# Performance work log

Measured on AMD Instinct MI355X. Metric: run time of the kernel, lower is better.

The kernel has to match this reference:

```python
import jax, jax.numpy as jnp
import numpy as np

N, E, NG = 10000, 160000, 64
HID, HEADS = 256, 4
NEG_SLOPE = 0.2


def setup_inputs() -> dict:
    key = jax.random.key(0)
    ks = jax.random.split(key, 20)
    s = 0.1
    inp = {
        "atom_features": jax.random.normal(ks[0], (N, 23), jnp.float32),
        "edge_index": jax.random.randint(ks[1], (2, E), 0, N),
        "batch": jnp.sort(jax.random.randint(ks[2], (N,), 0, NG)),
        "W1": jax.random.normal(ks[3], (23, HEADS * HID), jnp.float32) * s,
        "as1": jax.random.normal(ks[4], (HEADS, HID), jnp.float32) * s,
        "ad1": jax.random.normal(ks[5], (HEADS, HID), jnp.float32) * s,
        "b1": jnp.zeros((HEADS * HID,), jnp.float32),
        "W2": jax.random.normal(ks[6], (HEADS * HID, HEADS * HID), jnp.float32) * s,
        "as2": jax.random.normal(ks[7], (HEADS, HID), jnp.float32) * s,
        "ad2": jax.random.normal(ks[8], (HEADS, HID), jnp.float32) * s,
        "b2": jnp.zeros((HEADS * HID,), jnp.float32),
        "W3": jax.random.normal(ks[9], (HEADS * HID, HID), jnp.float32) * s,
        "as3": jax.random.normal(ks[10], (1, HID), jnp.float32) * s,
        "ad3": jax.random.normal(ks[11], (1, HID), jnp.float32) * s,
        "b3": jnp.zeros((HID,), jnp.float32),
        # MLP head
        "fc1_w": jax.random.normal(ks[12], (HID, HID // 2), jnp.float32) * s,
        "fc1_b": jnp.zeros((HID // 2,), jnp.float32),
        "fc2_w": jax.random.normal(ks[13], (HID // 2, 1), jnp.float32) * s,
        "fc2_b": jnp.zeros((1,), jnp.float32),
    }
    return inp


def gat_layer(x, W, att_src, att_dst, bias, src, dst, heads, ch):
    n = x.shape[0]
    h = (x @ W).reshape(n, heads, ch)                      # [N,H,C]
    a_s = jnp.sum(h * att_src, axis=-1)                    # [N,H]
    a_d = jnp.sum(h * att_dst, axis=-1)                    # [N,H]
    logits = jax.nn.leaky_relu(a_s[src] + a_d[dst], NEG_SLOPE)  # [E',H]
    m = jax.ops.segment_max(logits, dst, num_segments=n)
    m = jnp.where(jnp.isfinite(m), m, 0.0)
    e = jnp.exp(logits - m[dst])
    denom = jax.ops.segment_sum(e, dst, num_segments=n)
    alpha = e / (denom[dst] + 1e-16)                       # segment softmax over incoming edges
    out = jax.ops.segment_sum(alpha[:, :, None] * h[src], dst, num_segments=n)
    return out.reshape(n, heads * ch) + bias


def reference(atom_features, edge_index, batch,
              W1, as1, ad1, b1, W2, as2, ad2, b2, W3, as3, ad3, b3,
              fc1_w, fc1_b, fc2_w, fc2_b):
    n = atom_features.shape[0]
    loops = jnp.arange(n)
    src = jnp.concatenate([edge_index[0], loops])   # PyG GATConv adds self-loops
    dst = jnp.concatenate([edge_index[1], loops])

    x = jax.nn.elu(gat_layer(atom_features, W1, as1, ad1, b1, src, dst, HEADS, HID))
    x = jax.nn.elu(gat_layer(x, W2, as2, ad2, b2, src, dst, HEADS, HID))
    x = jax.nn.elu(gat_layer(x, W3, as3, ad3, b3, src, dst, 1, HID))
    # dropout: eval mode (training=False) -> identity

    # global mean pool over molecules
    sums = jax.ops.segment_sum(x, batch, num_segments=NG)
    counts = jax.ops.segment_sum(jnp.ones((n,), x.dtype), batch, num_segments=NG)
    features = sums / jnp.maximum(counts, 1.0)[:, None]    # [NG, HID]

    hmid = jax.nn.relu(features @ fc1_w + fc1_b)
    validity = hmid @ fc2_w + fc2_b                        # [NG, 1]
    return validity, features
```

## Files before the change

kernel.cpp:

```cpp
#include <hip/hip_runtime.h>
#include <hip/hip_bf16.h>
#include <math.h>

typedef unsigned short ushortT;
typedef __attribute__((ext_vector_type(8))) short short8;
typedef __attribute__((ext_vector_type(4))) float f32x4;

constexpr int NN   = 10000;
constexpr int EE   = 160000;
constexpr int ETOT = EE + NN;
constexpr int NG   = 64;
constexpr int HID  = 256;
constexpr int HEADS = 4;

__device__ __forceinline__ ushortT f2bf(float x) {
    __hip_bfloat16 h = __float2bfloat16(x);
    return *reinterpret_cast<ushortT*>(&h);
}
__device__ __forceinline__ float bf2f(ushortT x) {
    unsigned u = ((unsigned)x) << 16;
    return __uint_as_float(u);
}

__global__ void edge_count_kernel(const int* __restrict__ ei, int* __restrict__ cnt) {
    int e = blockIdx.x * blockDim.x + threadIdx.x;
    if (e >= ETOT) return;
    int dst = (e < EE) ? ei[EE + e] : (e - EE);
    atomicAdd(&cnt[dst], 1);
}

__global__ void scan_kernel(const int* __restrict__ cnt, int* __restrict__ row_ptr,
                            int* __restrict__ cursor) {
    __shared__ int part[256];
    int tid = threadIdx.x;
    const int chunk = (NN + 255) / 256;
    int s0 = tid * chunk;
    int s1 = min(NN, s0 + chunk);
    int sum = 0;
    for (int i = s0; i < s1; ++i) sum += cnt[i];
    part[tid] = sum;
    __syncthreads();
    for (int off = 1; off < 256; off <<= 1) {
        int v = (tid >= off) ? part[tid - off] : 0;
        __syncthreads();
        part[tid] += v;
        __syncthreads();
    }
    int run = (tid == 0) ? 0 : part[tid - 1];
    for (int i = s0; i < s1; ++i) {
        row_ptr[i] = run;
        cursor[i]  = run;
        run += cnt[i];
    }
    if (tid == 255) row_ptr[NN] = part[255];
}

__global__ void edge_fill_kernel(const int* __restrict__ ei, int* __restrict__ cursor,
                                 int* __restrict__ col_src) {
    int e = blockIdx.x * blockDim.x + threadIdx.x;
    if (e >= ETOT) return;
    int src, dst;
    if (e < EE) { src = ei[e]; dst = ei[EE + e]; }
    else        { src = dst = e - EE; }
    int pos = atomicAdd(&cursor[dst], 1);
    col_src[pos] = src;
}

__global__ void convert_wt(const float* __restrict__ W, ushortT* __restrict__ Wt,
                           int K, int N, int Kp) {
    __shared__ float t[32][33];
    int n0 = blockIdx.x * 32, k0 = blockIdx.y * 32;
    int tx = threadIdx.x, ty = threadIdx.y;
    for (int i = ty; i < 32; i += 8) {
        int k = k0 + i, n = n0 + tx;
        t[i][tx] = (k < K && n < N) ? W[(size_t)k * N + n] : 0.f;
    }
    __syncthreads();
    for (int i = ty; i < 32; i += 8) {
        int n = n0 + i, kp = k0 + tx;
        if (n < N && kp < Kp) Wt[(size_t)n * Kp + kp] = f2bf(t[tx][i]);
    }
}

__global__ void build_b1p(const float* __restrict__ W1, ushortT* __restrict__ Bp) {
    int idx = blockIdx.x * 256 + threadIdx.x;
    if (idx >= 1024 * 128) return;
    int n = idx >> 7, kp = idx & 127;
    int h = n >> 8, hk = kp >> 5, k = kp & 31;
    float v = (hk == h && k < 23) ? W1[(size_t)k * 1024 + n] : 0.f;
    Bp[idx] = f2bf(v);
}

__global__ void proj_att(const float* __restrict__ W,
                         const float* __restrict__ atts,
                         const float* __restrict__ attd,
                         float* __restrict__ wsv,
                         int K, int heads) {
    const int nout = 2 * heads;
    int gw   = (blockIdx.x * blockDim.x + threadIdx.x) >> 6;
    int lane = threadIdx.x & 63;
    if (gw >= K * nout) return;
    int k = gw / nout, o = gw - k * nout;
    int h = (o >= heads) ? (o - heads) : o;
    const float* att  = ((o >= heads) ? attd : atts) + h * HID;
    const float* wrow = W + (size_t)k * (heads * HID) + h * HID;
    float4 w4 = *(const float4*)(wrow + lane * 4);
    float4 a4 = *(const float4*)(att + lane * 4);
    float s = w4.x * a4.x + w4.y * a4.y + w4.z * a4.z + w4.w * a4.w;
    #pragma unroll
    for (int off = 1; off < 64; off <<= 1) s += __shfl_xor(s, off);
    if (lane == 0) wsv[(size_t)k * nout + o] = s;
}

__global__ void dots1_kernel(const float* __restrict__ atom,
                             const float* __restrict__ wsv1,
                             float* __restrict__ a_s, float* __restrict__ a_d) {
    int n = blockIdx.x * 256 + threadIdx.x;
    if (n >= NN) return;
    float a[8] = {0.f, 0.f, 0.f, 0.f, 0.f, 0.f, 0.f, 0.f};
    #pragma unroll
    for (int k = 0; k < 23; ++k) {
        float x = atom[n * 23 + k];
        #pragma unroll
        for (int o = 0; o < 8; ++o) a[o] += x * wsv1[k * 8 + o];
    }
    #pragma unroll
    for (int h = 0; h < 4; ++h) { a_s[n * 4 + h] = a[h]; a_d[n * 4 + h] = a[4 + h]; }
}

__global__ void dots2_kernel(const ushortT* __restrict__ x,
                             const float* __restrict__ wsv,
                             float* __restrict__ a_s, float* __restrict__ a_d) {
    int gw = (blockIdx.x * 256 + threadIdx.x) >> 6;
    int lane = threadIdx.x & 63;
    if (gw >= NN) return;
    const ushortT* row = x + (size_t)gw * 1024 + lane * 16;
    short8 v0 = *(const short8*)row;
    short8 v1 = *(const short8*)(row + 8);
    float ps[8] = {0.f, 0.f, 0.f, 0.f, 0.f, 0.f, 0.f, 0.f};
    const float* wb = wsv + (size_t)lane * 16 * 8;
    #pragma unroll
    for (int c = 0; c < 8; ++c) {
        float xv = bf2f((ushortT)v0[c]);
        #pragma unroll
        for (int o = 0; o < 8; ++o) ps[o] += xv * wb[c * 8 + o];
    }
    #pragma unroll
    for (int c = 0; c < 8; ++c) {
        float xv = bf2f((ushortT)v1[c]);
        #pragma unroll
        for (int o = 0; o < 8; ++o) ps[o] += xv * wb[(8 + c) * 8 + o];
    }
    #pragma unroll
    for (int off = 1; off < 64; off <<= 1) {
        #pragma unroll
        for (int o = 0; o < 8; ++o) ps[o] += __shfl_xor(ps[o], off);
    }
    if (lane == 0) {
        #pragma unroll
        for (int h = 0; h < 4; ++h) { a_s[gw * 4 + h] = ps[h]; a_d[gw * 4 + h] = ps[4 + h]; }
    }
}

__global__ __launch_bounds__(256) void agg_atom_kernel(const float* __restrict__ atom,
                                                       const float* __restrict__ a_s,
                                                       const float* __restrict__ a_d,
                                                       const int* __restrict__ rowp,
                                                       const int* __restrict__ colv,
                                                       ushortT* __restrict__ Ap) {
    int gw = (blockIdx.x * 256 + threadIdx.x) >> 6;
    int lane = threadIdx.x & 63;
    if (gw >= NN) return;
    const int i = gw;
    const int half = lane >> 5, c = lane & 31;
    const int start = rowp[i], end = rowp[i + 1];
    float4 ad4 = *(const float4*)(a_d + (size_t)i * 4);

    float acc[4] = {0.f, 0.f, 0.f, 0.f};
    float den[4] = {0.f, 0.f, 0.f, 0.f};
    for (int e0 = start; e0 < end; e0 += 2) {
        int e = e0 + half;
        bool val = (e < end);
        int s = colv[val ? e : e0];
        float x = (val && c < 23) ? atom[(size_t)s * 23 + c] : 0.f;
        float4 as4 = *(const float4*)(a_s + (size_t)s * 4);
        float l0 = as4.x + ad4.x; l0 = (l0 >= 0.f) ? l0 : 0.2f * l0;
        float l1 = as4.y + ad4.y; l1 = (l1 >= 0.f) ? l1 : 0.2f * l1;
        float l2 = as4.z + ad4.z; l2 = (l2 >= 0.f) ? l2 : 0.2f * l2;
        float l3 = as4.w + ad4.w; l3 = (l3 >= 0.f) ? l3 : 0.2f * l3;
        float w0 = val ? expf(l0) : 0.f;
        float w1 = val ? expf(l1) : 0.f;
        float w2 = val ? expf(l2) : 0.f;
        float w3 = val ? expf(l3) : 0.f;
        den[0] += w0; den[1] += w1; den[2] += w2; den[3] += w3;
        acc[0] += w0 * x; acc[1] += w1 * x; acc[2] += w2 * x; acc[3] += w3 * x;
    }
    #pragma unroll
    for (int h = 0; h < 4; ++h) {
        acc[h] += __shfl_xor(acc[h], 32);
        den[h] += __shfl_xor(den[h], 32);
    }
    if (half == 0) {
        #pragma unroll
        for (int h = 0; h < 4; ++h) {
            float v = acc[h] / (den[h] + 1e-16f);
            Ap[(size_t)i * 128 + h * 32 + c] = f2bf(v);
        }
    }
}

__device__ __forceinline__ void gload_lds16(const ushortT* gsrc, ushortT* ldst) {
    __builtin_amdgcn_global_load_lds(
        (const __attribute__((address_space(1))) unsigned int*)gsrc,
        (__attribute__((address_space(3))) unsigned int*)ldst, 16, 0, 0);
}

template<int MODE>
__global__ __launch_bounds__(256, 2) void gemm_bf16(const ushortT* __restrict__ A,
                                                    const ushortT* __restrict__ Bt,
                                                    ushortT* __restrict__ C,
                                                    const float* __restrict__ bias,
                                                    int M, int N, int K) {
    __shared__ ushortT lds[2][2][128][32];
    const int tid  = threadIdx.x;
    const int lane = tid & 63, w = tid >> 6;
    const int wm = w >> 1, wn = w & 1;
    const int row0 = blockIdx.y * 128;
    const int col0 = blockIdx.x * 128;
    const int nt = K >> 5;

    auto stage = [&](int buf, int t) {
        int k0 = t << 5;
        #pragma unroll
        for (int i = 0; i < 2; ++i) {
            int gbase = (w * 2 + i) * 64;
            int g = gbase + lane;
            int row = g >> 2;
            int sw = (row & 3) ^ ((row >> 2) & 3);
            int koff = (g & 3) ^ sw;
            int arow = min(row0 + row, M - 1);
            gload_lds16(A + (size_t)arow * K + k0 + koff * 8,
                        &lds[buf][0][0][0] + gbase * 8);
            int brow = col0 + row;
            gload_lds16(Bt + (size_t)brow * K + k0 + koff * 8,
                        &lds[buf][1][0][0] + gbase * 8);
        }
    };

    f32x4 acc[4][4] = {};
    const int lr = lane & 15, lk = lane >> 4;

    stage(0, 0);
    for (int t = 0; t < nt; ++t) {
        int buf = t & 1;
        __syncthreads();
        if (t + 1 < nt) stage(buf ^ 1, t + 1);
        short8 a[4], b[4];
        const ushortT* baseA = &lds[buf][0][0][0];
        const ushortT* baseB = &lds[buf][1][0][0];
        #pragma unroll
        for (int m = 0; m < 4; ++m) {
            int row = wm * 64 + m * 16 + lr;
            int sw = (row & 3) ^ ((row >> 2) & 3);
            a[m] = *(const short8*)(baseA + row * 32 + ((lk ^ sw) * 8));
        }
        #pragma unroll
        for (int n = 0; n < 4; ++n) {
            int row = wn * 64 + n * 16 + lr;
            int sw = (row & 3) ^ ((row >> 2) & 3);
            b[n] = *(const short8*)(baseB + row * 32 + ((lk ^ sw) * 8));
        }
        #pragma unroll
        for (int m = 0; m < 4; ++m)
            #pragma unroll
            for (int n = 0; n < 4; ++n)
                acc[m][n] = __builtin_amdgcn_mfma_f32_16x16x32_bf16(a[m], b[n], acc[m][n], 0, 0, 0);
    }

    #pragma unroll
    for (int m = 0; m < 4; ++m) {
        #pragma unroll
        for (int n = 0; n < 4; ++n) {
            int col = col0 + wn * 64 + n * 16 + lr;
            float bv = (MODE == 1) ? bias[col] : 0.f;
            #pragma unroll
            for (int j = 0; j < 4; ++j) {
                int rowg = row0 + wm * 64 + m * 16 + lk * 4 + j;
                if (rowg < M) {
                    float v = acc[m][n][j];
                    if (MODE == 1) { v += bv; v = (v > 0.f) ? v : expm1f(v); }
                    C[(size_t)rowg * N + col] = f2bf(v);
                }
            }
        }
    }
}

__global__ __launch_bounds__(256) void gat_agg_h4(const ushortT* __restrict__ hfeat,
                                                  const float* __restrict__ a_s,
                                                  const float* __restrict__ a_d,
                                                  const int* __restrict__ rowp,
                                                  const int* __restrict__ colv,
                                                  const float* __restrict__ bias,
                                                  ushortT* __restrict__ out16,
                                                  const float* __restrict__ wsv3,
                                                  float* __restrict__ as3,
                                                  float* __restrict__ ad3) {
    const int wv = threadIdx.x >> 6, lane = threadIdx.x & 63;
    const int i = blockIdx.x * 4 + wv;
    if (i >= NN) return;
    const int c0 = lane * 16;
    const int hh = c0 >> 8;
    const int start = rowp[i], end = rowp[i + 1];

    __shared__ float wsh[4][64][4];
    __shared__ int   ssh[4][64];

    float acc[16];
    #pragma unroll
    for (int c = 0; c < 16; ++c) acc[c] = 0.f;
    float den4[4] = {0.f, 0.f, 0.f, 0.f};

    for (int cb = start; cb < end; cb += 64) {
        int clen = min(64, end - cb);
        if (lane < clen) {
            int s = colv[cb + lane];
            ssh[wv][lane] = s;
            float4 as4 = *(const float4*)(a_s + (size_t)s * 4);
            float4 ad4 = *(const float4*)(a_d + (size_t)i * 4);
            float l0 = as4.x + ad4.x; l0 = (l0 >= 0.f) ? l0 : 0.2f * l0;
            float l1 = as4.y + ad4.y; l1 = (l1 >= 0.f) ? l1 : 0.2f * l1;
            float l2 = as4.z + ad4.z; l2 = (l2 >= 0.f) ? l2 : 0.2f * l2;
            float l3 = as4.w + ad4.w; l3 = (l3 >= 0.f) ? l3 : 0.2f * l3;
            float w0 = expf(l0), w1 = expf(l1), w2 = expf(l2), w3 = expf(l3);
            *reinterpret_cast<float4*>(&wsh[wv][lane][0]) = make_float4(w0, w1, w2, w3);
            den4[0] += w0; den4[1] += w1; den4[2] += w2; den4[3] += w3;
        }
        __builtin_amdgcn_wave_barrier();
        for (int e = 0; e < clen; ++e) {
            int s = ssh[wv][e];
            float wgt = wsh[wv][e][hh];
            const ushortT* p = hfeat + (size_t)s * 1024 + c0;
            short8 v0 = *(const short8*)p;
            short8 v1 = *(const short8*)(p + 8);
            #pragma unroll
            for (int j = 0; j < 8; ++j) {
                acc[j]     += wgt * bf2f((ushortT)v0[j]);
                acc[8 + j] += wgt * bf2f((ushortT)v1[j]);
            }
        }
        __builtin_amdgcn_wave_barrier();
    }

    #pragma unroll
    for (int off = 1; off < 64; off <<= 1) {
        den4[0] += __shfl_xor(den4[0], off);
        den4[1] += __shfl_xor(den4[1], off);
        den4[2] += __shfl_xor(den4[2], off);
        den4[3] += __shfl_xor(den4[3], off);
    }
    float den = (hh == 0) ? den4[0] : (hh == 1) ? den4[1] : (hh == 2) ? den4[2] : den4[3];
    float inv = 1.f / (den + 1e-16f);

    float vout[16];
    ushortT pk[16];
    #pragma unroll
    for (int c = 0; c < 16; ++c) {
        float v = acc[c] * inv + bias[c0 + c];
        v = (v > 0.f) ? v : expm1f(v);
        vout[c] = v;
        pk[c] = f2bf(v);
    }
    *reinterpret_cast<short8*>(out16 + (size_t)i * 1024 + c0)     = *reinterpret_cast<short8*>(&pk[0]);
    *reinterpret_cast<short8*>(out16 + (size_t)i * 1024 + c0 + 8) = *reinterpret_cast<short8*>(&pk[8]);

    float p0 = 0.f, p1 = 0.f;
    #pragma unroll
    for (int c = 0; c < 16; ++c) {
        float2 w2 = *(const float2*)(wsv3 + (size_t)(c0 + c) * 2);
        p0 += vout[c] * w2.x;
        p1 += vout[c] * w2.y;
    }
    #pragma unroll
    for (int off = 1; off < 64; off <<= 1) {
        p0 += __shfl_xor(p0, off);
        p1 += __shfl_xor(p1, off);
    }
    if (lane == 0) { as3[i] = p0; ad3[i] = p1; }
}

__global__ __launch_bounds__(256) void gat_agg_h1(const ushortT* __restrict__ hfeat,
                                                  const float* __restrict__ a_s,
                                                  const float* __restrict__ a_d,
                                                  const int* __restrict__ rowp,
                                                  const int* __restrict__ colv,
                                                  const float* __restrict__ bias,
                                                  float* __restrict__ outf) {
    const int wv = threadIdx.x >> 6, lane = threadIdx.x & 63;
    const int i = blockIdx.x * 4 + wv;
    if (i >= NN) return;
    const int c0 = lane * 4;
    const int start = rowp[i], end = rowp[i + 1];
    const float adi = a_d[i];

    __shared__ float wsh[4][64];
    __shared__ int   ssh[4][64];

    float acc[4] = {0.f, 0.f, 0.f, 0.f};
    float den = 0.f;

    for (int cb = start; cb < end; cb += 64) {
        int clen = min(64, end - cb);
        if (lane < clen) {
            int s = colv[cb + lane];
            ssh[wv][lane] = s;
            float l = a_s[s] + adi;
            l = (l >= 0.f) ? l : 0.2f * l;
            float w0 = expf(l);
            wsh[wv][lane] = w0;
            den += w0;
        }
        __builtin_amdgcn_wave_barrier();
        for (int e = 0; e < clen; ++e) {
            int s = ssh[wv][e];
            float wgt = wsh[wv][e];
            ushort4 v = *(const ushort4*)(hfeat + (size_t)s * 256 + c0);
            acc[0] += wgt * bf2f(v.x); acc[1] += wgt * bf2f(v.y);
            acc[2] += wgt * bf2f(v.z); acc[3] += wgt * bf2f(v.w);
        }
        __builtin_amdgcn_wave_barrier();
    }

    #pragma unroll
    for (int off = 1; off < 64; off <<= 1) den += __shfl_xor(den, off);
    float inv = 1.f / (den + 1e-16f);

    float4 o4;
    float v0 = acc[0] * inv + bias[c0 + 0]; o4.x = (v0 > 0.f) ? v0 : expm1f(v0);
    float v1 = acc[1] * inv + bias[c0 + 1]; o4.y = (v1 > 0.f) ? v1 : expm1f(v1);
    float v2 = acc[2] * inv + bias[c0 + 2]; o4.z = (v2 > 0.f) ? v2 : expm1f(v2);
    float v3 = acc[3] * inv + bias[c0 + 3]; o4.w = (v3 > 0.f) ? v3 : expm1f(v3);
    *reinterpret_cast<float4*>(outf + (size_t)i * 256 + c0) = o4;
}

__global__ void pool_mlp(const float* __restrict__ x,
                         const int* __restrict__ batch,
                         const float* __restrict__ fc1_w,
                         const float* __restrict__ fc1_b,
                         const float* __restrict__ fc2_w,
                         const float* __restrict__ fc2_b,
                         float* __restrict__ out) {
    int g = blockIdx.x, tid = threadIdx.x;
    int lo = 0, hi = NN;
    while (lo < hi) { int mid = (lo + hi) >> 1; if (batch[mid] < g) lo = mid + 1; else hi = mid; }
    int s0 = lo;
    lo = 0; hi = NN;
    while (lo < hi) { int mid = (lo + hi) >> 1; if (batch[mid] < g + 1) lo = mid + 1; else hi = mid; }
    int s1 = lo;

    float acc = 0.f;
    for (int n = s0; n < s1; ++n) acc += x[(size_t)n * HID + tid];
    float cnt = (float)(s1 - s0);
    float feat = acc / fmaxf(cnt, 1.f);
    out[NG + g * HID + tid] = feat;

    __shared__ float fsh[HID];
    fsh[tid] = feat;
    __syncthreads();
    __shared__ float r2[128];
    if (tid < 128) {
        float a = fc1_b[tid];
        for (int c = 0; c < HID; ++c) a += fsh[c] * fc1_w[c * 128 + tid];
        a = fmaxf(a, 0.f);
        r2[tid] = a * fc2_w[tid];
    }
    __syncthreads();
    for (int s2 = 64; s2 > 0; s2 >>= 1) {
        if (tid < s2) r2[tid] += r2[tid + s2];
        __syncthreads();
    }
    if (tid == 0) out[g] = r2[0] + fc2_b[0];
}

extern "C" void kernel_launch(void* const* d_in, const int* in_sizes, int n_in,
                              void* d_out, int out_size, void* d_ws, size_t ws_size,
                              hipStream_t stream) {
    const float* atom  = (const float*)d_in[0];
    const int*   ei    = (const int*)  d_in[1];
    const int*   batch = (const int*)  d_in[2];
    const float* W1  = (const float*)d_in[3];
    const float* as1 = (const float*)d_in[4];
    const float* ad1 = (const float*)d_in[5];
    const float* b1  = (const float*)d_in[6];
    const float* W2  = (const float*)d_in[7];
    const float* as2 = (const float*)d_in[8];
    const float* ad2 = (const float*)d_in[9];
    const float* b2  = (const float*)d_in[10];
    const float* W3  = (const float*)d_in[11];
    const float* as3 = (const float*)d_in[12];
    const float* ad3 = (const float*)d_in[13];
    const float* b3  = (const float*)d_in[14];
    const float* fc1w = (const float*)d_in[15];
    const float* fc1b = (const float*)d_in[16];
    const float* fc2w = (const float*)d_in[17];
    const float* fc2b = (const float*)d_in[18];
    float* out = (float*)d_out;

    ushortT* h16  = (ushortT*)d_ws;
    ushortT* x16  = h16 + (size_t)NN * 1024;
    ushortT* Ap   = x16 + (size_t)NN * 1024;
    ushortT* b1p  = Ap + (size_t)NN * 128;
    ushortT* wt2  = b1p + 1024 * 128;
    ushortT* wt3  = wt2 + 1024 * 1024;
    float*   x3   = (float*)(wt3 + 256 * 1024);
    float*   asL1 = x3 + (size_t)NN * 256;
    float*   adL1 = asL1 + (size_t)NN * 4;
    float*   asL2 = adL1 + (size_t)NN * 4;
    float*   adL2 = asL2 + (size_t)NN * 4;
    float*   asL3 = adL2 + (size_t)NN * 4;
    float*   adL3 = asL3 + NN;
    float*   wsv1 = adL3 + NN;
    float*   wsv2 = wsv1 + 23 * 8;
    float*   wsv3 = wsv2 + 1024 * 8;
    int*   cnt    = (int*)(wsv3 + 1024 * 2);
    int*   rowp   = cnt + NN;
    int*   cursor = rowp + NN + 1;
    int*   col    = cursor + NN;

    hipMemsetAsync(cnt, 0, NN * sizeof(int), stream);
    edge_count_kernel<<<(ETOT + 255) / 256, 256, 0, stream>>>(ei, cnt);
    scan_kernel<<<1, 256, 0, stream>>>(cnt, rowp, cursor);
    edge_fill_kernel<<<(ETOT + 255) / 256, 256, 0, stream>>>(ei, cursor, col);

    dim3 cblk(32, 8);
    convert_wt<<<dim3(32, 32), cblk, 0, stream>>>(W2, wt2, 1024, 1024, 1024);
    convert_wt<<<dim3(8, 32),  cblk, 0, stream>>>(W3, wt3, 1024, 256,  1024);
    build_b1p<<<(1024 * 128 + 255) / 256, 256, 0, stream>>>(W1, b1p);
    proj_att<<<(23 * 8 * 64 + 255) / 256, 256, 0, stream>>>(W1, as1, ad1, wsv1, 23, 4);
    proj_att<<<(1024 * 8 * 64 + 255) / 256, 256, 0, stream>>>(W2, as2, ad2, wsv2, 1024, 4);
    proj_att<<<(1024 * 2 * 64 + 255) / 256, 256, 0, stream>>>(W3, as3, ad3, wsv3, 1024, 1);

    dim3 blk(256);
    const int gy   = (NN + 127) / 128;
    const int gagg = (NN + 3) / 4;
    const int gwav = (NN * 64 + 255) / 256;

    dots1_kernel<<<(NN + 255) / 256, blk, 0, stream>>>(atom, wsv1, asL1, adL1);
    agg_atom_kernel<<<gwav, blk, 0, stream>>>(atom, asL1, adL1, rowp, col, Ap);
    gemm_bf16<1><<<dim3(8, gy), blk, 0, stream>>>(Ap, b1p, x16, b1, NN, 1024, 128);

    dots2_kernel<<<gwav, blk, 0, stream>>>(x16, wsv2, asL2, adL2);
    gemm_bf16<0><<<dim3(8, gy), blk, 0, stream>>>(x16, wt2, h16, nullptr, NN, 1024, 1024);
    gat_agg_h4<<<gagg, blk, 0, stream>>>(h16, asL2, adL2, rowp, col, b2, x16, wsv3, asL3, adL3);

    gemm_bf16<0><<<dim3(2, gy), blk, 0, stream>>>(x16, wt3, h16, nullptr, NN, 256, 1024);
    gat_agg_h1<<<gagg, blk, 0, stream>>>(h16, asL3, adL3, rowp, col, b3, x3);

    pool_mlp<<<NG, blk, 0, stream>>>(x3, batch, fc1w, fc1b, fc2w, fc2b, out);
}
```

Baseline: 341.2 us.

## Merge setup kernels, XCD-swizzle GEMM blocks, unroll gathers, split layer-3 dots

Several unrelated changes. The two weight-transpose launches become one 3D-grid kernel, and the three attention-projection launches become one. The GEMM remaps block indices so neighbouring tiles land on the same XCD for L2 locality. The gather loops in both aggregation kernels are unrolled by four to keep more loads in flight. agg_atom is rewritten to stage edge weights in LDS and process edges in chunks. The layer-3 attention dot products move out of the h4 aggregation epilogue into a separate dots3 kernel, which adds a launch and an extra read of x16 but lightens the aggregation kernel.

```diff
diff --git a/kernel.cpp b/kernel.cpp
--- a/kernel.cpp
+++ b/kernel.cpp
@@ -20,6 +20,12 @@
 __device__ __forceinline__ float bf2f(ushortT x) {
     unsigned u = ((unsigned)x) << 16;
     return __uint_as_float(u);
+}
+
+__device__ __forceinline__ int xcd_swz(int flat, int nwg) {
+    int q = nwg >> 3, r = nwg & 7;
+    int xcd = flat & 7, j = flat >> 3;
+    return (xcd < r ? xcd * (q + 1) : r * (q + 1) + (xcd - r) * q) + j;
 }
 
 __global__ void edge_count_kernel(const int* __restrict__ ei, int* __restrict__ cnt) {
@@ -66,8 +72,12 @@
     col_src[pos] = src;
 }
 
-__global__ void convert_wt(const float* __restrict__ W, ushortT* __restrict__ Wt,
-                           int K, int N, int Kp) {
+__global__ void convert_wt2(const float* __restrict__ W2, ushortT* __restrict__ wt2,
+                            const float* __restrict__ W3, ushortT* __restrict__ wt3) {
+    const float* W; ushortT* Wt; int N;
+    if (blockIdx.z == 0) { W = W2; Wt = wt2; N = 1024; }
+    else                 { W = W3; Wt = wt3; N = 256; if (blockIdx.x >= 8) return; }
+    const int K = 1024, Kp = 1024;
     __shared__ float t[32][33];
     int n0 = blockIdx.x * 32, k0 = blockIdx.y * 32;
     int tx = threadIdx.x, ty = threadIdx.y;
@@ -91,16 +101,21 @@
     Bp[idx] = f2bf(v);
 }
 
-__global__ void proj_att(const float* __restrict__ W,
-                         const float* __restrict__ atts,
-                         const float* __restrict__ attd,
-                         float* __restrict__ wsv,
-                         int K, int heads) {
+__global__ void proj_all(const float* __restrict__ W1, const float* __restrict__ as1,
+                         const float* __restrict__ ad1, float* __restrict__ wsv1,
+                         const float* __restrict__ W2, const float* __restrict__ as2,
+                         const float* __restrict__ ad2, float* __restrict__ wsv2,
+                         const float* __restrict__ W3, const float* __restrict__ as3,
+                         const float* __restrict__ ad3, float* __restrict__ wsv3) {
+    int gw   = (blockIdx.x * 256 + threadIdx.x) >> 6;
+    int lane = threadIdx.x & 63;
+    const float *W, *atts, *attd; float* wsv; int heads, idx;
+    if (gw < 23 * 8)               { W = W1; atts = as1; attd = ad1; wsv = wsv1; heads = 4; idx = gw; }
+    else if (gw < 23 * 8 + 8192)   { W = W2; atts = as2; attd = ad2; wsv = wsv2; heads = 4; idx = gw - 184; }
+    else if (gw < 23 * 8 + 8192 + 2048) { W = W3; atts = as3; attd = ad3; wsv = wsv3; heads = 1; idx = gw - 184 - 8192; }
+    else return;
     const int nout = 2 * heads;
-    int gw   = (blockIdx.x * blockDim.x + threadIdx.x) >> 6;
-    int lane = threadIdx.x & 63;
-    if (gw >= K * nout) return;
-    int k = gw / nout, o = gw - k * nout;
+    int k = idx / nout, o = idx - k * nout;
     int h = (o >= heads) ? (o - heads) : o;
     const float* att  = ((o >= heads) ? attd : atts) + h * HID;
     const float* wrow = W + (size_t)k * (heads * HID) + h * HID;
@@ -162,165 +177,54 @@
     }
 }
 
+__global__ void dots3_kernel(const ushortT* __restrict__ x,
+                             const float* __restrict__ wsv,
+                             float* __restrict__ a_s, float* __restrict__ a_d) {
+    int gw = (blockIdx.x * 256 + threadIdx.x) >> 6;
+    int lane = threadIdx.x & 63;
+    if (gw >= NN) return;
+    const ushortT* row = x + (size_t)gw * 1024 + lane * 16;
+    short8 v0 = *(const short8*)row;
+    short8 v1 = *(const short8*)(row + 8);
+    float p0 = 0.f, p1 = 0.f;
+    const int c0 = lane * 16;
+    #pragma unroll
+    for (int c = 0; c < 8; ++c) {
+        float xv = bf2f((ushortT)v0[c]);
+        float2 w2 = *(const float2*)(wsv + (size_t)(c0 + c) * 2);
+        p0 += xv * w2.x; p1 += xv * w2.y;
+    }
+    #pragma unroll
+    for (int c = 0; c < 8; ++c) {
+        float xv = bf2f((ushortT)v1[c]);
+        float2 w2 = *(const float2*)(wsv + (size_t)(c0 + 8 + c) * 2);
+        p0 += xv * w2.x; p1 += xv * w2.y;
+    }
+    #pragma unroll
+    for (int off = 1; off < 64; off <<= 1) {
+        p0 += __shfl_xor(p0, off);
+        p1 += __shfl_xor(p1, off);
+    }
+    if (lane == 0) { a_s[gw] = p0; a_d[gw] = p1; }
+}
+
 __global__ __launch_bounds__(256) void agg_atom_kernel(const float* __restrict__ atom,
                                                        const float* __restrict__ a_s,
                                                        const float* __restrict__ a_d,
                                                        const int* __restrict__ rowp,
                                                        const int* __restrict__ colv,
                                                        ushortT* __restrict__ Ap) {
-    int gw = (blockIdx.x * 256 + threadIdx.x) >> 6;
-    int lane = threadIdx.x & 63;
-    if (gw >= NN) return;
-    const int i = gw;
-    const int half = lane >> 5, c = lane & 31;
-    const int start = rowp[i], end = rowp[i + 1];
-    float4 ad4 = *(const float4*)(a_d + (size_t)i * 4);
-
-    float acc[4] = {0.f, 0.f, 0.f, 0.f};
-    float den[4] = {0.f, 0.f, 0.f, 0.f};
-    for (int e0 = start; e0 < end; e0 += 2) {
-        int e = e0 + half;
-        bool val = (e < end);
-        int s = colv[val ? e : e0];
-        float x = (val && c < 23) ? atom[(size_t)s * 23 + c] : 0.f;
-        float4 as4 = *(const float4*)(a_s + (size_t)s * 4);
-        float l0 = as4.x + ad4.x; l0 = (l0 >= 0.f) ? l0 : 0.2f * l0;
-        float l1 = as4.y + ad4.y; l1 = (l1 >= 0.f) ? l1 : 0.2f * l1;
-        float l2 = as4.z + ad4.z; l2 = (l2 >= 0.f) ? l2 : 0.2f * l2;
-        float l3 = as4.w + ad4.w; l3 = (l3 >= 0.f) ? l3 : 0.2f * l3;
-        float w0 = val ? expf(l0) : 0.f;
-        float w1 = val ? expf(l1) : 0.f;
-        float w2 = val ? expf(l2) : 0.f;
-        float w3 = val ? expf(l3) : 0.f;
-        den[0] += w0; den[1] += w1; den[2] += w2; den[3] += w3;
-        acc[0] += w0 * x; acc[1] += w1 * x; acc[2] += w2 * x; acc[3] += w3 * x;
-    }
-    #pragma unroll
-    for (int h = 0; h < 4; ++h) {
-        acc[h] += __shfl_xor(acc[h], 32);
-        den[h] += __shfl_xor(den[h], 32);
-    }
-    if (half == 0) {
-        #pragma unroll
-        for (int h = 0; h < 4; ++h) {
-            float v = acc[h] / (den[h] + 1e-16f);
-            Ap[(size_t)i * 128 + h * 32 + c] = f2bf(v);
-        }
-    }
-}
-
-__device__ __forceinline__ void gload_lds16(const ushortT* gsrc, ushortT* ldst) {
-    __builtin_amdgcn_global_load_lds(
-        (const __attribute__((address_space(1))) unsigned int*)gsrc,
-        (__attribute__((address_space(3))) unsigned int*)ldst, 16, 0, 0);
-}
-
-template<int MODE>
-__global__ __launch_bounds__(256, 2) void gemm_bf16(const ushortT* __restrict__ A,
-                                                    const ushortT* __restrict__ Bt,
-                                                    ushortT* __restrict__ C,
-                                                    const float* __restrict__ bias,
-                                                    int M, int N, int K) {
-    __shared__ ushortT lds[2][2][128][32];
-    const int tid  = threadIdx.x;
-    const int lane = tid & 63, w = tid >> 6;
-    const int wm = w >> 1, wn = w & 1;
-    const int row0 = blockIdx.y * 128;
-    const int col0 = blockIdx.x * 128;
-    const int nt = K >> 5;
-
-    auto stage = [&](int buf, int t) {
-        int k0 = t << 5;
-        #pragma unroll
-        for (int i = 0; i < 2; ++i) {
-            int gbase = (w * 2 + i) * 64;
-            int g = gbase + lane;
-            int row = g >> 2;
-            int sw = (row & 3) ^ ((row >> 2) & 3);
-            int koff = (g & 3) ^ sw;
-            int arow = min(row0 + row, M - 1);
-            gload_lds16(A + (size_t)arow * K + k0 + koff * 8,
-                        &lds[buf][0][0][0] + gbase * 8);
-            int brow = col0 + row;
-            gload_lds16(Bt + (size_t)brow * K + k0 + koff * 8,
-                        &lds[buf][1][0][0] + gbase * 8);
-        }
-    };
-
-    f32x4 acc[4][4] = {};
-    const int lr = lane & 15, lk = lane >> 4;
-
-    stage(0, 0);
-    for (int t = 0; t < nt; ++t) {
-        int buf = t & 1;
-        __syncthreads();
-        if (t + 1 < nt) stage(buf ^ 1, t + 1);
-        short8 a[4], b[4];
-        const ushortT* baseA = &lds[buf][0][0][0];
-        const ushortT* baseB = &lds[buf][1][0][0];
-        #pragma unroll
-        for (int m = 0; m < 4; ++m) {
-            int row = wm * 64 + m * 16 + lr;
-            int sw = (row & 3) ^ ((row >> 2) & 3);
-            a[m] = *(const short8*)(baseA + row * 32 + ((lk ^ sw) * 8));
-        }
-        #pragma unroll
-        for (int n = 0; n < 4; ++n) {
-            int row = wn * 64 + n * 16 + lr;
-            int sw = (row & 3) ^ ((row >> 2) & 3);
-            b[n] = *(const short8*)(baseB + row * 32 + ((lk ^ sw) * 8));
-        }
-        #pragma unroll
-        for (int m = 0; m < 4; ++m)
-            #pragma unroll
-            for (int n = 0; n < 4; ++n)
-                acc[m][n] = __builtin_amdgcn_mfma_f32_16x16x32_bf16(a[m], b[n], acc[m][n], 0, 0, 0);
-    }
-
-    #pragma unroll
-    for (int m = 0; m < 4; ++m) {
-        #pragma unroll
-        for (int n = 0; n < 4; ++n) {
-            int col = col0 + wn * 64 + n * 16 + lr;
-            float bv = (MODE == 1) ? bias[col] : 0.f;
-            #pragma unroll
-            for (int j = 0; j < 4; ++j) {
-                int rowg = row0 + wm * 64 + m * 16 + lk * 4 + j;
-                if (rowg < M) {
-                    float v = acc[m][n][j];
-                    if (MODE == 1) { v += bv; v = (v > 0.f) ? v : expm1f(v); }
-                    C[(size_t)rowg * N + col] = f2bf(v);
-                }
-            }
-        }
-    }
-}
-
-__global__ __launch_bounds__(256) void gat_agg_h4(const ushortT* __restrict__ hfeat,
-                                                  const float* __restrict__ a_s,
-                                                  const float* __restrict__ a_d,
-                                                  const int* __restrict__ rowp,
-                                                  const int* __restrict__ colv,
-                                                  const float* __restrict__ bias,
-                                                  ushortT* __restrict__ out16,
-                                                  const float* __restrict__ wsv3,
-                                                  float* __restrict__ as3,
-                                                  float* __restrict__ ad3) {
     const int wv = threadIdx.x >> 6, lane = threadIdx.x & 63;
     const int i = blockIdx.x * 4 + wv;
     if (i >= NN) return;
-    const int c0 = lane * 16;
-    const int hh = c0 >> 8;
+    const int half = lane >> 5, c = lane & 31;
     const int start = rowp[i], end = rowp[i + 1];
 
     __shared__ float wsh[4][64][4];
     __shared__ int   ssh[4][64];
 
-    float acc[16];
-    #pragma unroll
-    for (int c = 0; c < 16; ++c) acc[c] = 0.f;
+    float acc[4] = {0.f, 0.f, 0.f, 0.f};
     float den4[4] = {0.f, 0.f, 0.f, 0.f};
-
     for (int cb = start; cb < end; cb += 64) {
         int clen = min(64, end - cb);
         if (lane < clen) {
@@ -337,7 +241,185 @@
             den4[0] += w0; den4[1] += w1; den4[2] += w2; den4[3] += w3;
         }
         __builtin_amdgcn_wave_barrier();
-        for (int e = 0; e < clen; ++e) {
+        for (int e = half; e < clen; e += 2) {
+            int s = ssh[wv][e];
+            float x = (c < 23) ? atom[(size_t)s * 23 + c] : 0.f;
+            acc[0] += wsh[wv][e][0] * x;
+            acc[1] += wsh[wv][e][1] * x;
+            acc[2] += wsh[wv][e][2] * x;
+            acc[3] += wsh[wv][e][3] * x;
+        }
+        __builtin_amdgcn_wave_barrier();
+    }
+    #pragma unroll
+    for (int h = 0; h < 4; ++h) acc[h] += __shfl_xor(acc[h], 32);
+    #pragma unroll
+    for (int off = 1; off < 64; off <<= 1) {
+        den4[0] += __shfl_xor(den4[0], off);
+        den4[1] += __shfl_xor(den4[1], off);
+        den4[2] += __shfl_xor(den4[2], off);
+        den4[3] += __shfl_xor(den4[3], off);
+    }
+    if (half == 0) {
+        #pragma unroll
+        for (int h = 0; h < 4; ++h) {
+            float v = acc[h] / (den4[h] + 1e-16f);
+            Ap[(size_t)i * 128 + h * 32 + c] = f2bf(v);
+        }
+    }
+}
+
+__device__ __forceinline__ void gload_lds16(const ushortT* gsrc, ushortT* ldst) {
+    __builtin_amdgcn_global_load_lds(
+        (const __attribute__((address_space(1))) unsigned int*)gsrc,
+        (__attribute__((address_space(3))) unsigned int*)ldst, 16, 0, 0);
+}
+
+template<int MODE>
+__global__ __launch_bounds__(256, 2) void gemm_bf16(const ushortT* __restrict__ A,
+                                                    const ushortT* __restrict__ Bt,
+                                                    ushortT* __restrict__ C,
+                                                    const float* __restrict__ bias,
+                                                    int M, int N, int K) {
+    __shared__ ushortT lds[2][2][128][32];
+    const int tid  = threadIdx.x;
+    const int lane = tid & 63, w = tid >> 6;
+    const int wm = w >> 1, wn = w & 1;
+    const int nwg  = gridDim.x * gridDim.y;
+    const int flat = blockIdx.y * gridDim.x + blockIdx.x;
+    const int swz  = xcd_swz(flat, nwg);
+    const int bx = swz % gridDim.x, by = swz / gridDim.x;
+    const int row0 = by * 128;
+    const int col0 = bx * 128;
+    const int nt = K >> 5;
+
+    auto stage = [&](int buf, int t) {
+        int k0 = t << 5;
+        #pragma unroll
+        for (int i = 0; i < 2; ++i) {
+            int gbase = (w * 2 + i) * 64;
+            int g = gbase + lane;
+            int row = g >> 2;
+            int sw = (row & 3) ^ ((row >> 2) & 3);
+            int koff = (g & 3) ^ sw;
+            int arow = min(row0 + row, M - 1);
+            gload_lds16(A + (size_t)arow * K + k0 + koff * 8,
+                        &lds[buf][0][0][0] + gbase * 8);
+            int brow = col0 + row;
+            gload_lds16(Bt + (size_t)brow * K + k0 + koff * 8,
+                        &lds[buf][1][0][0] + gbase * 8);
+        }
+    };
+
+    f32x4 acc[4][4] = {};
+    const int lr = lane & 15, lk = lane >> 4;
+
+    stage(0, 0);
+    for (int t = 0; t < nt; ++t) {
+        int buf = t & 1;
+        __syncthreads();
+        if (t + 1 < nt) stage(buf ^ 1, t + 1);
+        short8 a[4], b[4];
+        const ushortT* baseA = &lds[buf][0][0][0];
+        const ushortT* baseB = &lds[buf][1][0][0];
+        #pragma unroll
+        for (int m = 0; m < 4; ++m) {
+            int row = wm * 64 + m * 16 + lr;
+            int sw = (row & 3) ^ ((row >> 2) & 3);
+            a[m] = *(const short8*)(baseA + row * 32 + ((lk ^ sw) * 8));
+        }
+        #pragma unroll
+        for (int n = 0; n < 4; ++n) {
+            int row = wn * 64 + n * 16 + lr;
+            int sw = (row & 3) ^ ((row >> 2) & 3);
+            b[n] = *(const short8*)(baseB + row * 32 + ((lk ^ sw) * 8));
+        }
+        #pragma unroll
+        for (int m = 0; m < 4; ++m)
+            #pragma unroll
+            for (int n = 0; n < 4; ++n)
+                acc[m][n] = __builtin_amdgcn_mfma_f32_16x16x32_bf16(a[m], b[n], acc[m][n], 0, 0, 0);
+    }
+
+    #pragma unroll
+    for (int m = 0; m < 4; ++m) {
+        #pragma unroll
+        for (int n = 0; n < 4; ++n) {
+            int col = col0 + wn * 64 + n * 16 + lr;
+            float bv = (MODE == 1) ? bias[col] : 0.f;
+            #pragma unroll
+            for (int j = 0; j < 4; ++j) {
+                int rowg = row0 + wm * 64 + m * 16 + lk * 4 + j;
+                if (rowg < M) {
+                    float v = acc[m][n][j];
+                    if (MODE == 1) { v += bv; v = (v > 0.f) ? v : expm1f(v); }
+                    C[(size_t)rowg * N + col] = f2bf(v);
+                }
+            }
+        }
+    }
+}
+
+__global__ __launch_bounds__(256) void gat_agg_h4(const ushortT* __restrict__ hfeat,
+                                                  const float* __restrict__ a_s,
+                                                  const float* __restrict__ a_d,
+                                                  const int* __restrict__ rowp,
+                                                  const int* __restrict__ colv,
+                                                  const float* __restrict__ bias,
+                                                  ushortT* __restrict__ out16) {
+    const int wv = threadIdx.x >> 6, lane = threadIdx.x & 63;
+    const int i = blockIdx.x * 4 + wv;
+    if (i >= NN) return;
+    const int c0 = lane * 16;
+    const int hh = c0 >> 8;
+    const int start = rowp[i], end = rowp[i + 1];
+
+    __shared__ float wsh[4][64][4];
+    __shared__ int   ssh[4][64];
+
+    float acc[16];
+    #pragma unroll
+    for (int c = 0; c < 16; ++c) acc[c] = 0.f;
+    float den4[4] = {0.f, 0.f, 0.f, 0.f};
+
+    for (int cb = start; cb < end; cb += 64) {
+        int clen = min(64, end - cb);
+        if (lane < clen) {
+            int s = colv[cb + lane];
+            ssh[wv][lane] = s;
+            float4 as4 = *(const float4*)(a_s + (size_t)s * 4);
+            float4 ad4 = *(const float4*)(a_d + (size_t)i * 4);
+            float l0 = as4.x + ad4.x; l0 = (l0 >= 0.f) ? l0 : 0.2f * l0;
+            float l1 = as4.y + ad4.y; l1 = (l1 >= 0.f) ? l1 : 0.2f * l1;
+            float l2 = as4.z + ad4.z; l2 = (l2 >= 0.f) ? l2 : 0.2f * l2;
+            float l3 = as4.w + ad4.w; l3 = (l3 >= 0.f) ? l3 : 0.2f * l3;
+            float w0 = expf(l0), w1 = expf(l1), w2 = expf(l2), w3 = expf(l3);
+            *reinterpret_cast<float4*>(&wsh[wv][lane][0]) = make_float4(w0, w1, w2, w3);
+            den4[0] += w0; den4[1] += w1; den4[2] += w2; den4[3] += w3;
+        }
+        __builtin_amdgcn_wave_barrier();
+        int e = 0;
+        for (; e + 4 <= clen; e += 4) {
+            int sa = ssh[wv][e], sb = ssh[wv][e + 1], sc = ssh[wv][e + 2], sd = ssh[wv][e + 3];
+            const ushortT* pa = hfeat + (size_t)sa * 1024 + c0;
+            const ushortT* pb = hfeat + (size_t)sb * 1024 + c0;
+            const ushortT* pc = hfeat + (size_t)sc * 1024 + c0;
+            const ushortT* pd = hfeat + (size_t)sd * 1024 + c0;
+            short8 va0 = *(const short8*)pa,       va1 = *(const short8*)(pa + 8);
+            short8 vb0 = *(const short8*)pb,       vb1 = *(const short8*)(pb + 8);
+            short8 vc0 = *(const short8*)pc,       vc1 = *(const short8*)(pc + 8);
+            short8 vd0 = *(const short8*)pd,       vd1 = *(const short8*)(pd + 8);
+            float wa = wsh[wv][e][hh],     wb = wsh[wv][e + 1][hh];
+            float wc = wsh[wv][e + 2][hh], wd = wsh[wv][e + 3][hh];
+            #pragma unroll
+            for (int j = 0; j < 8; ++j) {
+                acc[j]     += wa * bf2f((ushortT)va0[j]) + wb * bf2f((ushortT)vb0[j])
+                            + wc * bf2f((ushortT)vc0[j]) + wd * bf2f((ushortT)vd0[j]);
+                acc[8 + j] += wa * bf2f((ushortT)va1[j]) + wb * bf2f((ushortT)vb1[j])
+                            + wc * bf2f((ushortT)vc1[j]) + wd * bf2f((ushortT)vd1[j]);
+            }
+        }
+        for (; e < clen; ++e) {
             int s = ssh[wv][e];
             float wgt = wsh[wv][e][hh];
             const ushortT* p = hfeat + (size_t)s * 1024 + c0;
@@ -362,31 +444,15 @@
     float den = (hh == 0) ? den4[0] : (hh == 1) ? den4[1] : (hh == 2) ? den4[2] : den4[3];
     float inv = 1.f / (den + 1e-16f);
 
-    float vout[16];
     ushortT pk[16];
     #pragma unroll
     for (int c = 0; c < 16; ++c) {
         float v = acc[c] * inv + bias[c0 + c];
         v = (v > 0.f) ? v : expm1f(v);
-        vout[c] = v;
         pk[c] = f2bf(v);
     }
     *reinterpret_cast<short8*>(out16 + (size_t)i * 1024 + c0)     = *reinterpret_cast<short8*>(&pk[0]);
     *reinterpret_cast<short8*>(out16 + (size_t)i * 1024 + c0 + 8) = *reinterpret_cast<short8*>(&pk[8]);
-
-    float p0 = 0.f, p1 = 0.f;
-    #pragma unroll
-    for (int c = 0; c < 16; ++c) {
-        float2 w2 = *(const float2*)(wsv3 + (size_t)(c0 + c) * 2);
-        p0 += vout[c] * w2.x;
-        p1 += vout[c] * w2.y;
-    }
-    #pragma unroll
-    for (int off = 1; off < 64; off <<= 1) {
-        p0 += __shfl_xor(p0, off);
-        p1 += __shfl_xor(p1, off);
-    }
-    if (lane == 0) { as3[i] = p0; ad3[i] = p1; }
 }
 
 __global__ __launch_bounds__(256) void gat_agg_h1(const ushortT* __restrict__ hfeat,
@@ -421,7 +487,20 @@
             den += w0;
         }
         __builtin_amdgcn_wave_barrier();
-        for (int e = 0; e < clen; ++e) {
+        int e = 0;
+        for (; e + 4 <= clen; e += 4) {
+            int sa = ssh[wv][e], sb = ssh[wv][e + 1], sc = ssh[wv][e + 2], sd = ssh[wv][e + 3];
+            ushort4 va = *(const ushort4*)(hfeat + (size_t)sa * 256 + c0);
+            ushort4 vb = *(const ushort4*)(hfeat + (size_t)sb * 256 + c0);
+            ushort4 vc = *(const ushort4*)(hfeat + (size_t)sc * 256 + c0);
+            ushort4 vd = *(const ushort4*)(hfeat + (size_t)sd * 256 + c0);
+            float wa = wsh[wv][e], wb2 = wsh[wv][e + 1], wc2 = wsh[wv][e + 2], wd2 = wsh[wv][e + 3];
+            acc[0] += wa * bf2f(va.x) + wb2 * bf2f(vb.x) + wc2 * bf2f(vc.x) + wd2 * bf2f(vd.x);
+            acc[1] += wa * bf2f(va.y) + wb2 * bf2f(vb.y) + wc2 * bf2f(vc.y) + wd2 * bf2f(vd.y);
+            acc[2] += wa * bf2f(va.z) + wb2 * bf2f(vb.z) + wc2 * bf2f(vc.z) + wd2 * bf2f(vd.z);
+            acc[3] += wa * bf2f(va.w) + wb2 * bf2f(vb.w) + wc2 * bf2f(vc.w) + wd2 * bf2f(vd.w);
+        }
+        for (; e < clen; ++e) {
             int s = ssh[wv][e];
             float wgt = wsh[wv][e];
             ushort4 v = *(const ushort4*)(hfeat + (size_t)s * 256 + c0);
@@ -532,27 +611,24 @@
     scan_kernel<<<1, 256, 0, stream>>>(cnt, rowp, cursor);
     edge_fill_kernel<<<(ETOT + 255) / 256, 256, 0, stream>>>(ei, cursor, col);
 
-    dim3 cblk(32, 8);
-    convert_wt<<<dim3(32, 32), cblk, 0, stream>>>(W2, wt2, 1024, 1024, 1024);
-    convert_wt<<<dim3(8, 32),  cblk, 0, stream>>>(W3, wt3, 1024, 256,  1024);
+    convert_wt2<<<dim3(32, 32, 2), dim3(32, 8), 0, stream>>>(W2, wt2, W3, wt3);
     build_b1p<<<(1024 * 128 + 255) / 256, 256, 0, stream>>>(W1, b1p);
-    proj_att<<<(23 * 8 * 64 + 255) / 256, 256, 0, stream>>>(W1, as1, ad1, wsv1, 23, 4);
-    proj_att<<<(1024 * 8 * 64 + 255) / 256, 256, 0, stream>>>(W2, as2, ad2, wsv2, 1024, 4);
-    proj_att<<<(1024 * 2 * 64 + 255) / 256, 256, 0, stream>>>(W3, as3, ad3, wsv3, 1024, 1);
+    proj_all<<<((23 * 8 + 8192 + 2048) * 64 + 255) / 256, 256, 0, stream>>>(
+        W1, as1, ad1, wsv1, W2, as2, ad2, wsv2, W3, as3, ad3, wsv3);
 
     dim3 blk(256);
     const int gy   = (NN + 127) / 128;
     const int gagg = (NN + 3) / 4;
-    const int gwav = (NN * 64 + 255) / 256;
 
     dots1_kernel<<<(NN + 255) / 256, blk, 0, stream>>>(atom, wsv1, asL1, adL1);
-    agg_atom_kernel<<<gwav, blk, 0, stream>>>(atom, asL1, adL1, rowp, col, Ap);
+    agg_atom_kernel<<<gagg, blk, 0, stream>>>(atom, asL1, adL1, rowp, col, Ap);
     gemm_bf16<1><<<dim3(8, gy), blk, 0, stream>>>(Ap, b1p, x16, b1, NN, 1024, 128);
 
-    dots2_kernel<<<gwav, blk, 0, stream>>>(x16, wsv2, asL2, adL2);
+    dots2_kernel<<<gagg, blk, 0, stream>>>(x16, wsv2, asL2, adL2);
     gemm_bf16<0><<<dim3(8, gy), blk, 0, stream>>>(x16, wt2, h16, nullptr, NN, 1024, 1024);
-    gat_agg_h4<<<gagg, blk, 0, stream>>>(h16, asL2, adL2, rowp, col, b2, x16, wsv3, asL3, adL3);
-
+    gat_agg_h4<<<gagg, blk, 0, stream>>>(h16, asL2, adL2, rowp, col, b2, x16);
+
+    dots3_kernel<<<gagg, blk, 0, stream>>>(x16, wsv3, asL3, adL3);
     gemm_bf16<0><<<dim3(2, gy), blk, 0, stream>>>(x16, wt3, h16, nullptr, NN, 256, 1024);
     gat_agg_h1<<<gagg, blk, 0, stream>>>(h16, asL3, adL3, rowp, col, b3, x3);
 
```

Result: faster. 324.1 us (-5.0%).
